# Performance work log

Measured on AMD Instinct MI355X. Metric: run time of the kernel, lower is better.

Reference implementation:

```python
import jax, jax.numpy as jnp
import numpy as np

EMBED_DIM = 1024
NUM_HEADS = 16
HEAD_DIM = EMBED_DIM // NUM_HEADS


def setup_inputs() -> dict:
    key = jax.random.key(0)
    ks = jax.random.split(key, 9)
    B, T, C = 2, 2048, EMBED_DIM
    s = 1.0 / np.sqrt(C)
    return {
        "x": jax.random.normal(ks[0], (B, T, C), dtype=jnp.float32),
        "Wq": jax.random.normal(ks[1], (C, C), dtype=jnp.float32) * s,
        "bq": jnp.zeros((C,), dtype=jnp.float32),
        "Wk": jax.random.normal(ks[2], (C, C), dtype=jnp.float32) * s,
        "bk": jnp.zeros((C,), dtype=jnp.float32),
        "Wv": jax.random.normal(ks[3], (C, C), dtype=jnp.float32) * s,
        "bv": jnp.zeros((C,), dtype=jnp.float32),
        "Wo": jax.random.normal(ks[4], (C, C), dtype=jnp.float32) * s,
        "bo": jnp.zeros((C,), dtype=jnp.float32),
    }


def reference(x, Wq, bq, Wk, bk, Wv, bv, Wo, bo):
    B, T, C = x.shape
    H, D = NUM_HEADS, HEAD_DIM
    # projections (torch Linear: x @ W.T + b; here W stored as [in,out])
    q = (x @ Wq + bq).reshape(B, T, H, D).transpose(0, 2, 1, 3)  # [B,H,T,D]
    k = (x @ Wk + bk).reshape(B, T, H, D).transpose(0, 2, 1, 3)
    v = (x @ Wv + bv).reshape(B, T, H, D).transpose(0, 2, 1, 3)
    scores = jnp.einsum("bhtd,bhsd->bhts", q, k) / jnp.sqrt(jnp.float32(D))
    causal = jnp.tril(jnp.ones((T, T), dtype=bool))  # keep lower triangle
    scores = jnp.where(causal, scores, -jnp.inf)
    weights = jax.nn.softmax(scores, axis=-1)
    attended = jnp.einsum("bhts,bhsd->bhtd", weights, v)
    attended = attended.transpose(0, 2, 1, 3).reshape(B, T, C)
    return attended @ Wo + bo
```

## Files before the change

kernel.cpp:

```cpp
#include <hip/hip_runtime.h>
#include <math.h>


#define BLOCK 256

typedef __attribute__((ext_vector_type(8))) short bf16x8;
typedef __attribute__((ext_vector_type(4))) float f32x4;
typedef __attribute__((ext_vector_type(16))) float f32x16;

__device__ inline short f2bf(float f) {
  union { float f; unsigned u; } c; c.f = f;
  unsigned u = c.u;
  unsigned r = (u + 0x7fffu + ((u >> 16) & 1u)) >> 16;
  return (short)r;
}

#define GLD_LDS16(g, l)                                            \
  __builtin_amdgcn_global_load_lds(                                \
      (const __attribute__((address_space(1))) unsigned int*)(g),  \
      (__attribute__((address_space(3))) unsigned int*)(l), 16, 0, 0)


__global__ void cvt_x_kernel(const float* __restrict__ x, short* __restrict__ xb) {
  int i = (blockIdx.x * BLOCK + threadIdx.x) * 8;
  float4 a = *(const float4*)(x + i);
  float4 b = *(const float4*)(x + i + 4);
  alignas(16) short o[8];
  o[0] = f2bf(a.x); o[1] = f2bf(a.y); o[2] = f2bf(a.z); o[3] = f2bf(a.w);
  o[4] = f2bf(b.x); o[5] = f2bf(b.y); o[6] = f2bf(b.z); o[7] = f2bf(b.w);
  *(int4*)(xb + i) = *(int4*)o;
}

__global__ void cvt_w_kernel(const float* __restrict__ Wq, const float* __restrict__ Wk,
                             const float* __restrict__ Wv, const float* __restrict__ Wo,
                             short* __restrict__ Wtqkv, short* __restrict__ Wto) {
  __shared__ float tile[32][33];
  int z = blockIdx.z;
  const float* W = (z == 0) ? Wq : (z == 1) ? Wk : (z == 2) ? Wv : Wo;
  short* outp = (z == 3) ? Wto : (Wtqkv + (size_t)z * 1024 * 1024);
  int k0 = blockIdx.x * 32, n0 = blockIdx.y * 32;
  int tr = threadIdx.x >> 5, tc = threadIdx.x & 31;
#pragma unroll
  for (int i = 0; i < 4; i++)
    tile[tr + i * 8][tc] = W[(k0 + tr + i * 8) * 1024 + n0 + tc];
  __syncthreads();
#pragma unroll
  for (int i = 0; i < 4; i++)
    outp[(n0 + tr + i * 8) * 1024 + k0 + tc] = f2bf(tile[tc][tr + i * 8]);
}


__global__ __launch_bounds__(BLOCK) void gemm_qkv_kernel(
    const short* __restrict__ A, const short* __restrict__ Wt,
    const float* __restrict__ bq, const float* __restrict__ bk,
    const float* __restrict__ bv,
    short* __restrict__ Qo, short* __restrict__ Ko, short* __restrict__ Vo) {
  const int Kd = 1024;
  const float QSCL = 0.18033688011f;
  int m0 = blockIdx.x * 128, n0 = blockIdx.y * 128;
  int t = threadIdx.x;
  int lane = t & 63, wv = t >> 6;
  int quad = lane >> 4, lc = lane & 15;
  int wy = wv >> 1, wx = wv & 1;
  __shared__ short As[128 * 32];
  __shared__ short Bs[128 * 32];
  int r0 = t >> 2, c0 = (t & 3) * 8;
  f32x4 acc[4][4] = {};
  const short* Arow0 = A + (size_t)(m0 + r0) * Kd + c0;
  const short* Arow1 = A + (size_t)(m0 + r0 + 64) * Kd + c0;
  const short* Brow0 = Wt + (size_t)(n0 + r0) * Kd + c0;
  const short* Brow1 = Wt + (size_t)(n0 + r0 + 64) * Kd + c0;
  for (int k0 = 0; k0 < Kd; k0 += 32) {
    __syncthreads();
    GLD_LDS16(Arow0 + k0, &As[8 * t]);
    GLD_LDS16(Arow1 + k0, &As[8 * t + 2048]);
    GLD_LDS16(Brow0 + k0, &Bs[8 * t]);
    GLD_LDS16(Brow1 + k0, &Bs[8 * t + 2048]);
    __syncthreads();
    bf16x8 af[4], bf[4];
#pragma unroll
    for (int i = 0; i < 4; i++)
      af[i] = *(const bf16x8*)&As[(wy * 64 + i * 16 + lc) * 32 + quad * 8];
#pragma unroll
    for (int i = 0; i < 4; i++)
      bf[i] = *(const bf16x8*)&Bs[(wx * 64 + i * 16 + lc) * 32 + quad * 8];
#pragma unroll
    for (int mi = 0; mi < 4; mi++)
#pragma unroll
      for (int ni = 0; ni < 4; ni++)
        acc[mi][ni] = __builtin_amdgcn_mfma_f32_16x16x32_bf16(af[mi], bf[ni], acc[mi][ni], 0, 0, 0);
  }
#pragma unroll
  for (int mi = 0; mi < 4; mi++) {
    int row = m0 + wy * 64 + mi * 16 + quad * 4;
#pragma unroll
    for (int ni = 0; ni < 4; ni++) {
      int col = n0 + wx * 64 + ni * 16 + lc;
      int which = col >> 10;
      int hd = col & 1023;
      int h = hd >> 6, d = hd & 63;
      float bb = (which == 0) ? bq[hd] : (which == 1) ? bk[hd] : bv[hd];
      if (which == 2) {
        alignas(8) short pk[4];
#pragma unroll
        for (int r = 0; r < 4; r++) pk[r] = f2bf(acc[mi][ni][r] + bb);
        int b = row >> 11, tt = row & 2047;
        *(int2*)&Vo[((size_t)(b * 16 + h) * 64 + d) * 2048 + tt] = *(const int2*)pk;
      } else {
#pragma unroll
        for (int r = 0; r < 4; r++) {
          int rw = row + r;
          int b = rw >> 11, tt = rw & 2047;
          float val = acc[mi][ni][r] + bb;
          if (which == 0) {
            Qo[((size_t)(b * 16 + h) * 2048 + tt) * 64 + d] = f2bf(val * QSCL);
          } else {
            Ko[((size_t)(b * 16 + h) * 2048 + tt) * 64 + d] = f2bf(val);
          }
        }
      }
    }
  }
}


__global__ __launch_bounds__(BLOCK) void gemm_out_kernel(
    const short* __restrict__ A, const short* __restrict__ Wt,
    const float* __restrict__ bias, float* __restrict__ Out) {
  const int Kd = 1024;
  int m0 = blockIdx.x * 128, n0 = blockIdx.y * 128;
  int t = threadIdx.x;
  int lane = t & 63, wv = t >> 6;
  int quad = lane >> 4, lc = lane & 15;
  int wy = wv >> 1, wx = wv & 1;
  __shared__ short As[128 * 32];
  __shared__ short Bs[128 * 32];
  int r0 = t >> 2, c0 = (t & 3) * 8;
  f32x4 acc[4][4] = {};
  const short* Arow0 = A + (size_t)(m0 + r0) * Kd + c0;
  const short* Arow1 = A + (size_t)(m0 + r0 + 64) * Kd + c0;
  const short* Brow0 = Wt + (size_t)(n0 + r0) * Kd + c0;
  const short* Brow1 = Wt + (size_t)(n0 + r0 + 64) * Kd + c0;
  for (int k0 = 0; k0 < Kd; k0 += 32) {
    __syncthreads();
    GLD_LDS16(Arow0 + k0, &As[8 * t]);
    GLD_LDS16(Arow1 + k0, &As[8 * t + 2048]);
    GLD_LDS16(Brow0 + k0, &Bs[8 * t]);
    GLD_LDS16(Brow1 + k0, &Bs[8 * t + 2048]);
    __syncthreads();
    bf16x8 af[4], bf[4];
#pragma unroll
    for (int i = 0; i < 4; i++)
      af[i] = *(const bf16x8*)&As[(wy * 64 + i * 16 + lc) * 32 + quad * 8];
#pragma unroll
    for (int i = 0; i < 4; i++)
      bf[i] = *(const bf16x8*)&Bs[(wx * 64 + i * 16 + lc) * 32 + quad * 8];
#pragma unroll
    for (int mi = 0; mi < 4; mi++)
#pragma unroll
      for (int ni = 0; ni < 4; ni++)
        acc[mi][ni] = __builtin_amdgcn_mfma_f32_16x16x32_bf16(af[mi], bf[ni], acc[mi][ni], 0, 0, 0);
  }
#pragma unroll
  for (int mi = 0; mi < 4; mi++) {
    int row = m0 + wy * 64 + mi * 16 + quad * 4;
#pragma unroll
    for (int ni = 0; ni < 4; ni++) {
      int col = n0 + wx * 64 + ni * 16 + lc;
      float bb = bias[col];
#pragma unroll
      for (int r = 0; r < 4; r++)
        Out[(size_t)(row + r) * 1024 + col] = acc[mi][ni][r] + bb;
    }
  }
}


__global__ __launch_bounds__(BLOCK, 1) void attn_kernel(
    const short* __restrict__ Q, const short* __restrict__ K,
    const short* __restrict__ Vt, short* __restrict__ Oa) {
  int bh = blockIdx.x >> 3;
  int pair = blockIdx.x & 7;
  int t = threadIdx.x;
  int lane = t & 63, w = t >> 6;
  int ln = lane & 31, lh = lane >> 5;
  const short* Qb = Q + (size_t)bh * 2048 * 64;
  const short* Kb = K + (size_t)bh * 2048 * 64;
  const short* Vg = Vt + (size_t)bh * 64 * 2048;
  int b = bh >> 4, h = bh & 15;

  __shared__ short Kt[64 * 72];
  __shared__ short Vs[64 * 72];
  __shared__ short Ps[4][32 * 72];
  short* Pw = Ps[w];

  int srow = t >> 2;
  int scol = (t & 3) * 16;
  const float M2 = 14.5f;

  for (int sp = 0; sp < 2; sp++) {
    int s = sp ? (15 - pair) : pair;
    int q0 = s * 128;
    int q0w = q0 + w * 32;
    int ntiles = 2 * s + 2;
    int ntw = 2 * s + 1 + (w >> 1);

    bf16x8 qf[4];
#pragma unroll
    for (int c = 0; c < 4; c++)
      qf[c] = *(const bf16x8*)&Qb[(size_t)(q0w + ln) * 64 + c * 16 + lh * 8];

    f32x16 O0 = {}, O1 = {};
    float lsum = 0.f;

    int4 ka0 = *(const int4*)&Kb[(size_t)srow * 64 + scol];
    int4 ka1 = *(const int4*)&Kb[(size_t)srow * 64 + scol + 8];
    int4 va0 = *(const int4*)&Vg[(size_t)srow * 2048 + scol];
    int4 va1 = *(const int4*)&Vg[(size_t)srow * 2048 + scol + 8];
    __syncthreads();
    *(int4*)&Kt[srow * 72 + scol] = ka0;
    *(int4*)&Kt[srow * 72 + scol + 8] = ka1;
    *(int4*)&Vs[srow * 72 + scol] = va0;
    *(int4*)&Vs[srow * 72 + scol + 8] = va1;
    __syncthreads();

    for (int kt = 0; kt < ntiles; kt++) {
      bool more = (kt + 1 < ntiles);
      if (more) {
        int kb2 = (kt + 1) * 64;
        ka0 = *(const int4*)&Kb[(size_t)(kb2 + srow) * 64 + scol];
        ka1 = *(const int4*)&Kb[(size_t)(kb2 + srow) * 64 + scol + 8];
        va0 = *(const int4*)&Vg[(size_t)srow * 2048 + kb2 + scol];
        va1 = *(const int4*)&Vg[(size_t)srow * 2048 + kb2 + scol + 8];
      }
      if (kt < ntw) {
        int kbase = kt * 64;
        f32x16 S[2] = {};
#pragma unroll
        for (int c = 0; c < 4; c++) {
          bf16x8 k0 = *(const bf16x8*)&Kt[ln * 72 + c * 16 + lh * 8];
          bf16x8 k1 = *(const bf16x8*)&Kt[(32 + ln) * 72 + c * 16 + lh * 8];
          S[0] = __builtin_amdgcn_mfma_f32_32x32x16_bf16(k0, qf[c], S[0], 0, 0, 0);
          S[1] = __builtin_amdgcn_mfma_f32_32x32x16_bf16(k1, qf[c], S[1], 0, 0, 0);
        }
        if (kt == ntw - 1) {
          int qg = q0w + ln;
#pragma unroll
          for (int kh = 0; kh < 2; kh++)
#pragma unroll
            for (int reg = 0; reg < 16; reg++) {
              int key = kbase + kh * 32 + (reg & 3) + 8 * (reg >> 2) + 4 * lh;
              if (key > qg) S[kh][reg] = -3.0e38f;
            }
        }
#pragma unroll
        for (int kh = 0; kh < 2; kh++)
#pragma unroll
          for (int g = 0; g < 4; g++) {
            unsigned u[4];
#pragma unroll
            for (int i = 0; i < 4; i++) {
              union { float f; unsigned v; } cc;
              cc.f = __builtin_amdgcn_exp2f(S[kh][g * 4 + i] - M2);
              lsum += cc.f;
              u[i] = cc.v + 0x8000u;
            }
            int2 pk;
            pk.x = (int)__builtin_amdgcn_perm(u[1], u[0], 0x07060302);
            pk.y = (int)__builtin_amdgcn_perm(u[3], u[2], 0x07060302);
            *(int2*)&Pw[ln * 72 + kh * 32 + g * 8 + lh * 4] = pk;
          }
#pragma unroll
        for (int c = 0; c < 4; c++) {
          bf16x8 pf = *(const bf16x8*)&Pw[ln * 72 + c * 16 + lh * 8];
          bf16x8 v0 = *(const bf16x8*)&Vs[ln * 72 + c * 16 + lh * 8];
          bf16x8 v1 = *(const bf16x8*)&Vs[(32 + ln) * 72 + c * 16 + lh * 8];
          O0 = __builtin_amdgcn_mfma_f32_32x32x16_bf16(v0, pf, O0, 0, 0, 0);
          O1 = __builtin_amdgcn_mfma_f32_32x32x16_bf16(v1, pf, O1, 0, 0, 0);
        }
      }
      if (more) {
        __syncthreads();
        *(int4*)&Kt[srow * 72 + scol] = ka0;
        *(int4*)&Kt[srow * 72 + scol + 8] = ka1;
        *(int4*)&Vs[srow * 72 + scol] = va0;
        *(int4*)&Vs[srow * 72 + scol + 8] = va1;
        __syncthreads();
      }
    }

    float lt = lsum + __shfl_xor(lsum, 32, 64);
    float inv = 1.0f / lt;
    size_t rowbase = (size_t)(b * 2048 + q0w + ln) * 1024 + h * 64;
#pragma unroll
    for (int dh = 0; dh < 2; dh++)
#pragma unroll
      for (int g = 0; g < 4; g++) {
        alignas(8) short pk[4];
#pragma unroll
        for (int i = 0; i < 4; i++) {
          float v = dh ? O1[g * 4 + i] : O0[g * 4 + i];
          pk[i] = f2bf(v * inv);
        }
        *(int2*)&Oa[rowbase + dh * 32 + g * 8 + lh * 4] = *(const int2*)pk;
      }
  }
}


extern "C" void kernel_launch(void* const* d_in, const int* in_sizes, int n_in,
                              void* d_out, int out_size, void* d_ws, size_t ws_size,
                              hipStream_t stream) {
  const float* x = (const float*)d_in[0];
  const float* Wq = (const float*)d_in[1];
  const float* bq = (const float*)d_in[2];
  const float* Wk = (const float*)d_in[3];
  const float* bk = (const float*)d_in[4];
  const float* Wv = (const float*)d_in[5];
  const float* bv = (const float*)d_in[6];
  const float* Wo = (const float*)d_in[7];
  const float* bo = (const float*)d_in[8];
  char* ws = (char*)d_ws;
  const size_t MB = 1024 * 1024;
  short* xb = (short*)(ws);
  short* Wtqkv = (short*)(ws + 8 * MB);
  short* Wto = (short*)(ws + 14 * MB);
  short* Qb = (short*)(ws + 17 * MB);
  short* Kb = (short*)(ws + 25 * MB);
  short* Vb = (short*)(ws + 33 * MB);
  short* Att = (short*)(ws + 41 * MB);
  float* out = (float*)d_out;

  cvt_x_kernel<<<2048, BLOCK, 0, stream>>>(x, xb);
  cvt_w_kernel<<<dim3(32, 32, 4), BLOCK, 0, stream>>>(Wq, Wk, Wv, Wo, Wtqkv, Wto);
  gemm_qkv_kernel<<<dim3(32, 24), BLOCK, 0, stream>>>(xb, Wtqkv, bq, bk, bv, Qb, Kb, Vb);
  attn_kernel<<<256, BLOCK, 0, stream>>>(Qb, Kb, Vb, Att);
  gemm_out_kernel<<<dim3(32, 8), BLOCK, 0, stream>>>(Att, Wto, bo, out);
}
```

Measured before the change: 199.5 us.

## Split attention keys across warps, shrink out-GEMM tile, widen QKV K-step

The attention kernel now processes 64-query tiles instead of 128, using 512 blocks at two blocks per CU. Warp pairs split the key tiles by parity and reduce their partial O and row sums through shared memory before writing. The output GEMM uses 64-row tiles so its grid doubles, and the QKV GEMM loads two 32-wide K slices per barrier pair to halve synchronisation. The cost is more shared-memory reduction traffic in attention, the need for more registers to fit two blocks per CU, and K/V being loaded more often across blocks.

```diff
diff --git a/kernel.cpp b/kernel.cpp
--- a/kernel.cpp
+++ b/kernel.cpp
@@ -62,33 +62,40 @@
   int lane = t & 63, wv = t >> 6;
   int quad = lane >> 4, lc = lane & 15;
   int wy = wv >> 1, wx = wv & 1;
-  __shared__ short As[128 * 32];
-  __shared__ short Bs[128 * 32];
+  __shared__ short As[2][128 * 32];
+  __shared__ short Bs[2][128 * 32];
   int r0 = t >> 2, c0 = (t & 3) * 8;
   f32x4 acc[4][4] = {};
   const short* Arow0 = A + (size_t)(m0 + r0) * Kd + c0;
   const short* Arow1 = A + (size_t)(m0 + r0 + 64) * Kd + c0;
   const short* Brow0 = Wt + (size_t)(n0 + r0) * Kd + c0;
   const short* Brow1 = Wt + (size_t)(n0 + r0 + 64) * Kd + c0;
-  for (int k0 = 0; k0 < Kd; k0 += 32) {
-    __syncthreads();
-    GLD_LDS16(Arow0 + k0, &As[8 * t]);
-    GLD_LDS16(Arow1 + k0, &As[8 * t + 2048]);
-    GLD_LDS16(Brow0 + k0, &Bs[8 * t]);
-    GLD_LDS16(Brow1 + k0, &Bs[8 * t + 2048]);
-    __syncthreads();
-    bf16x8 af[4], bf[4];
-#pragma unroll
-    for (int i = 0; i < 4; i++)
-      af[i] = *(const bf16x8*)&As[(wy * 64 + i * 16 + lc) * 32 + quad * 8];
-#pragma unroll
-    for (int i = 0; i < 4; i++)
-      bf[i] = *(const bf16x8*)&Bs[(wx * 64 + i * 16 + lc) * 32 + quad * 8];
-#pragma unroll
-    for (int mi = 0; mi < 4; mi++)
-#pragma unroll
-      for (int ni = 0; ni < 4; ni++)
-        acc[mi][ni] = __builtin_amdgcn_mfma_f32_16x16x32_bf16(af[mi], bf[ni], acc[mi][ni], 0, 0, 0);
+  for (int k0 = 0; k0 < Kd; k0 += 64) {
+    __syncthreads();
+    GLD_LDS16(Arow0 + k0, &As[0][8 * t]);
+    GLD_LDS16(Arow1 + k0, &As[0][8 * t + 2048]);
+    GLD_LDS16(Arow0 + k0 + 32, &As[1][8 * t]);
+    GLD_LDS16(Arow1 + k0 + 32, &As[1][8 * t + 2048]);
+    GLD_LDS16(Brow0 + k0, &Bs[0][8 * t]);
+    GLD_LDS16(Brow1 + k0, &Bs[0][8 * t + 2048]);
+    GLD_LDS16(Brow0 + k0 + 32, &Bs[1][8 * t]);
+    GLD_LDS16(Brow1 + k0 + 32, &Bs[1][8 * t + 2048]);
+    __syncthreads();
+#pragma unroll
+    for (int p = 0; p < 2; p++) {
+      bf16x8 af[4], bf[4];
+#pragma unroll
+      for (int i = 0; i < 4; i++)
+        af[i] = *(const bf16x8*)&As[p][(wy * 64 + i * 16 + lc) * 32 + quad * 8];
+#pragma unroll
+      for (int i = 0; i < 4; i++)
+        bf[i] = *(const bf16x8*)&Bs[p][(wx * 64 + i * 16 + lc) * 32 + quad * 8];
+#pragma unroll
+      for (int mi = 0; mi < 4; mi++)
+#pragma unroll
+        for (int ni = 0; ni < 4; ni++)
+          acc[mi][ni] = __builtin_amdgcn_mfma_f32_16x16x32_bf16(af[mi], bf[ni], acc[mi][ni], 0, 0, 0);
+    }
   }
 #pragma unroll
   for (int mi = 0; mi < 4; mi++) {
@@ -128,42 +135,40 @@
     const short* __restrict__ A, const short* __restrict__ Wt,
     const float* __restrict__ bias, float* __restrict__ Out) {
   const int Kd = 1024;
-  int m0 = blockIdx.x * 128, n0 = blockIdx.y * 128;
+  int m0 = blockIdx.x * 64, n0 = blockIdx.y * 128;
   int t = threadIdx.x;
   int lane = t & 63, wv = t >> 6;
   int quad = lane >> 4, lc = lane & 15;
   int wy = wv >> 1, wx = wv & 1;
-  __shared__ short As[128 * 32];
+  __shared__ short As[64 * 32];
   __shared__ short Bs[128 * 32];
   int r0 = t >> 2, c0 = (t & 3) * 8;
-  f32x4 acc[4][4] = {};
+  f32x4 acc[2][4] = {};
   const short* Arow0 = A + (size_t)(m0 + r0) * Kd + c0;
-  const short* Arow1 = A + (size_t)(m0 + r0 + 64) * Kd + c0;
   const short* Brow0 = Wt + (size_t)(n0 + r0) * Kd + c0;
   const short* Brow1 = Wt + (size_t)(n0 + r0 + 64) * Kd + c0;
   for (int k0 = 0; k0 < Kd; k0 += 32) {
     __syncthreads();
     GLD_LDS16(Arow0 + k0, &As[8 * t]);
-    GLD_LDS16(Arow1 + k0, &As[8 * t + 2048]);
     GLD_LDS16(Brow0 + k0, &Bs[8 * t]);
     GLD_LDS16(Brow1 + k0, &Bs[8 * t + 2048]);
     __syncthreads();
-    bf16x8 af[4], bf[4];
-#pragma unroll
-    for (int i = 0; i < 4; i++)
-      af[i] = *(const bf16x8*)&As[(wy * 64 + i * 16 + lc) * 32 + quad * 8];
+    bf16x8 af[2], bf[4];
+#pragma unroll
+    for (int i = 0; i < 2; i++)
+      af[i] = *(const bf16x8*)&As[(wy * 32 + i * 16 + lc) * 32 + quad * 8];
 #pragma unroll
     for (int i = 0; i < 4; i++)
       bf[i] = *(const bf16x8*)&Bs[(wx * 64 + i * 16 + lc) * 32 + quad * 8];
 #pragma unroll
-    for (int mi = 0; mi < 4; mi++)
+    for (int mi = 0; mi < 2; mi++)
 #pragma unroll
       for (int ni = 0; ni < 4; ni++)
         acc[mi][ni] = __builtin_amdgcn_mfma_f32_16x16x32_bf16(af[mi], bf[ni], acc[mi][ni], 0, 0, 0);
   }
 #pragma unroll
-  for (int mi = 0; mi < 4; mi++) {
-    int row = m0 + wy * 64 + mi * 16 + quad * 4;
+  for (int mi = 0; mi < 2; mi++) {
+    int row = m0 + wy * 32 + mi * 16 + quad * 4;
 #pragma unroll
     for (int ni = 0; ni < 4; ni++) {
       int col = n0 + wx * 64 + ni * 16 + lc;
@@ -176,13 +181,14 @@
 }
 
 
-__global__ __launch_bounds__(BLOCK, 1) void attn_kernel(
+__global__ __launch_bounds__(BLOCK, 2) void attn_kernel(
     const short* __restrict__ Q, const short* __restrict__ K,
     const short* __restrict__ Vt, short* __restrict__ Oa) {
-  int bh = blockIdx.x >> 3;
-  int pair = blockIdx.x & 7;
+  int bh = blockIdx.x >> 4;
+  int pair = blockIdx.x & 15;
   int t = threadIdx.x;
   int lane = t & 63, w = t >> 6;
+  int qhalf = w & 1, par = w >> 1;
   int ln = lane & 31, lh = lane >> 5;
   const short* Qb = Q + (size_t)bh * 2048 * 64;
   const short* Kb = K + (size_t)bh * 2048 * 64;
@@ -191,7 +197,8 @@
 
   __shared__ short Kt[64 * 72];
   __shared__ short Vs[64 * 72];
-  __shared__ short Ps[4][32 * 72];
+  __shared__ __align__(16) short Ps[4][32 * 72];
+  __shared__ float lx[2][64];
   short* Pw = Ps[w];
 
   int srow = t >> 2;
@@ -199,11 +206,10 @@
   const float M2 = 14.5f;
 
   for (int sp = 0; sp < 2; sp++) {
-    int s = sp ? (15 - pair) : pair;
-    int q0 = s * 128;
-    int q0w = q0 + w * 32;
-    int ntiles = 2 * s + 2;
-    int ntw = 2 * s + 1 + (w >> 1);
+    int s = sp ? (31 - pair) : pair;
+    int q0 = s * 64;
+    int q0w = q0 + qhalf * 32;
+    int ntiles = s + 1;
 
     bf16x8 qf[4];
 #pragma unroll
@@ -233,7 +239,7 @@
         va0 = *(const int4*)&Vg[(size_t)srow * 2048 + kb2 + scol];
         va1 = *(const int4*)&Vg[(size_t)srow * 2048 + kb2 + scol + 8];
       }
-      if (kt < ntw) {
+      if ((kt & 1) == par) {
         int kbase = kt * 64;
         f32x16 S[2] = {};
 #pragma unroll
@@ -243,7 +249,7 @@
           S[0] = __builtin_amdgcn_mfma_f32_32x32x16_bf16(k0, qf[c], S[0], 0, 0, 0);
           S[1] = __builtin_amdgcn_mfma_f32_32x32x16_bf16(k1, qf[c], S[1], 0, 0, 0);
         }
-        if (kt == ntw - 1) {
+        if (kt == ntiles - 1) {
           int qg = q0w + ln;
 #pragma unroll
           for (int kh = 0; kh < 2; kh++)
@@ -289,21 +295,42 @@
       }
     }
 
-    float lt = lsum + __shfl_xor(lsum, 32, 64);
-    float inv = 1.0f / lt;
-    size_t rowbase = (size_t)(b * 2048 + q0w + ln) * 1024 + h * 64;
-#pragma unroll
-    for (int dh = 0; dh < 2; dh++)
-#pragma unroll
-      for (int g = 0; g < 4; g++) {
-        alignas(8) short pk[4];
-#pragma unroll
-        for (int i = 0; i < 4; i++) {
-          float v = dh ? O1[g * 4 + i] : O0[g * 4 + i];
-          pk[i] = f2bf(v * inv);
-        }
-        *(int2*)&Oa[rowbase + dh * 32 + g * 8 + lh * 4] = *(const int2*)pk;
-      }
+    float* ob = (float*)&Ps[0][0];
+    __syncthreads();
+    if (par == 1) {
+      float* obw = ob + qhalf * 2048;
+#pragma unroll
+      for (int dh = 0; dh < 2; dh++)
+#pragma unroll
+        for (int reg = 0; reg < 16; reg++)
+          obw[((dh * 16 + reg) * 2 + lh) * 32 + ln] = dh ? O1[reg] : O0[reg];
+      lx[qhalf][lane] = lsum;
+    }
+    __syncthreads();
+    if (par == 0) {
+      float* obw = ob + qhalf * 2048;
+#pragma unroll
+      for (int reg = 0; reg < 16; reg++) {
+        O0[reg] += obw[((0 * 16 + reg) * 2 + lh) * 32 + ln];
+        O1[reg] += obw[((1 * 16 + reg) * 2 + lh) * 32 + ln];
+      }
+      float lt = lsum + lx[qhalf][lane];
+      lt += __shfl_xor(lt, 32, 64);
+      float inv = 1.0f / lt;
+      size_t rowbase = (size_t)(b * 2048 + q0w + ln) * 1024 + h * 64;
+#pragma unroll
+      for (int dh = 0; dh < 2; dh++)
+#pragma unroll
+        for (int g = 0; g < 4; g++) {
+          alignas(8) short pk[4];
+#pragma unroll
+          for (int i = 0; i < 4; i++) {
+            float v = dh ? O1[g * 4 + i] : O0[g * 4 + i];
+            pk[i] = f2bf(v * inv);
+          }
+          *(int2*)&Oa[rowbase + dh * 32 + g * 8 + lh * 4] = *(const int2*)pk;
+        }
+    }
   }
 }
 
@@ -334,6 +361,6 @@
   cvt_x_kernel<<<2048, BLOCK, 0, stream>>>(x, xb);
   cvt_w_kernel<<<dim3(32, 32, 4), BLOCK, 0, stream>>>(Wq, Wk, Wv, Wo, Wtqkv, Wto);
   gemm_qkv_kernel<<<dim3(32, 24), BLOCK, 0, stream>>>(xb, Wtqkv, bq, bk, bv, Qb, Kb, Vb);
-  attn_kernel<<<256, BLOCK, 0, stream>>>(Qb, Kb, Vb, Att);
-  gemm_out_kernel<<<dim3(32, 8), BLOCK, 0, stream>>>(Att, Wto, bo, out);
-}
+  attn_kernel<<<512, BLOCK, 0, stream>>>(Qb, Kb, Vb, Att);
+  gemm_out_kernel<<<dim3(64, 8), BLOCK, 0, stream>>>(Att, Wto, bo, out);
+}
```

Result: no change. 197.8 us (-0.8%).
